# Kernel optimization log

Measured on AMD Instinct MI355X. Metric: run time of the kernel, lower is better.

The kernel has to match this reference:

```python
import jax, jax.numpy as jnp
from jax import lax
import numpy as np

BN_EPS = 1e-5


def conv_transpose2d(x, w, b, stride, pad):
    # torch ConvTranspose2d weight layout: (in, out, kH, kW)
    k = w.shape[2]
    wt = jnp.flip(w, (2, 3)).transpose(1, 0, 2, 3)  # (out, in, kH, kW)
    p = k - 1 - pad
    out = lax.conv_general_dilated(
        x, wt, window_strides=(1, 1), padding=[(p, p), (p, p)],
        lhs_dilation=(stride, stride),
        dimension_numbers=("NCHW", "OIHW", "NCHW"))
    return out + b[None, :, None, None]


def conv2d(x, w, b, pad):
    out = lax.conv_general_dilated(
        x, w, window_strides=(1, 1), padding=[(pad, pad), (pad, pad)],
        dimension_numbers=("NCHW", "OIHW", "NCHW"))
    return out + b[None, :, None, None]


def batchnorm2d(x, gamma, beta):
    # training-mode BN: batch statistics over (N, H, W), biased variance
    mean = jnp.mean(x, axis=(0, 2, 3), keepdims=True)
    var = jnp.mean((x - mean) ** 2, axis=(0, 2, 3), keepdims=True)
    xn = (x - mean) * lax.rsqrt(var + BN_EPS)
    return xn * gamma[None, :, None, None] + beta[None, :, None, None]


def setup_inputs():
    key = jax.random.key(0)
    ks = jax.random.split(key, 8)
    B = 4096
    return {
        "x": jax.random.randint(ks[0], (B,), 0, 60032, dtype=jnp.int32),
        "encoder_w": jax.random.normal(ks[1], (60032, 7 * 7 * 64), jnp.float32) * 0.02,
        "emb_w": jax.random.normal(ks[2], (512, 64), jnp.float32) * 0.02,
        "deconv1_w": jax.random.normal(ks[3], (64, 32, 4, 4), jnp.float32) * 0.03,
        "deconv1_b": jnp.zeros((32,), jnp.float32),
        "bn1_g": jnp.ones((32,), jnp.float32),
        "bn1_b": jnp.zeros((32,), jnp.float32),
        "deconv2_w": jax.random.normal(ks[4], (32, 16, 4, 4), jnp.float32) * 0.04,
        "deconv2_b": jnp.zeros((16,), jnp.float32),
        "bn2_g": jnp.ones((16,), jnp.float32),
        "bn2_b": jnp.zeros((16,), jnp.float32),
        "conv_w": jax.random.normal(ks[5], (1, 16, 3, 3), jnp.float32) * 0.08,
        "conv_b": jnp.zeros((1,), jnp.float32),
    }


def reference(x, encoder_w, emb_w, deconv1_w, deconv1_b, bn1_g, bn1_b,
              deconv2_w, deconv2_b, bn2_g, bn2_b, conv_w, conv_b):
    # encoder embedding lookup -> [B, 64, 7, 7]
    z_e_x = encoder_w[x].reshape(-1, 64, 7, 7)
    z = z_e_x.transpose(0, 2, 3, 1)  # [B, H, W, C]
    # squared L2 distances to codebook, computed without the [B,H,W,C,K] blowup:
    # ||z||^2 - 2 z.e + ||e||^2, identical math to the broadcast-pow-sum
    d = ((z ** 2).sum(-1, keepdims=True)
         - 2.0 * jnp.einsum("bhwc,kc->bhwk", z, emb_w)
         + (emb_w ** 2).sum(-1))  # [B, H, W, K]
    latents = jnp.argmin(d, axis=-1)  # [B, H, W]
    z_q_x = emb_w[latents].transpose(0, 3, 1, 2)  # [B, 64, 7, 7]
    # decoder
    h = jax.nn.relu(batchnorm2d(conv_transpose2d(z_q_x, deconv1_w, deconv1_b, 2, 1), bn1_g, bn1_b))
    h = jax.nn.relu(batchnorm2d(conv_transpose2d(h, deconv2_w, deconv2_b, 2, 1), bn2_g, bn2_b))
    x_tilde = jax.nn.sigmoid(conv2d(h, conv_w, conv_b, 1))  # [B, 1, 28, 28]
    return (x_tilde, z_e_x, z_q_x)
```

## Files before the change

kernel.cpp:

```cpp
#include <hip/hip_runtime.h>
#include <hip/hip_bf16.h>
#include <math.h>

#define BATCH   4096
#define CH      64
#define KCB     512

#define XT_N    (BATCH*784)
#define ZE_OFF  (XT_N)
#define ZQ_OFF  (XT_N + BATCH*3136)

#define WS_C1   0
#define WS_C2   51380224ULL
#define WS_ST   154140672ULL
#define WS_WF2  154141824ULL
#define WS_EF   154158208ULL
#define WS_EE   154289280ULL
#define WS_WF1  WS_C2

typedef __attribute__((ext_vector_type(8))) __bf16 bf16x8;
typedef __attribute__((ext_vector_type(4))) float f32x4;
union B8 { uint4 u; bf16x8 v; };

__device__ inline unsigned short f2bf(float f) {
    unsigned int u = __float_as_uint(f);
    u = u + 0x7fffu + ((u >> 16) & 1u);
    return (unsigned short)(u >> 16);
}
__device__ inline float bf2f(unsigned short h) {
    return __uint_as_float(((unsigned int)h) << 16);
}

__global__ void k_prep(const float* __restrict__ w1, const float* __restrict__ w2,
                       const float* __restrict__ emb,
                       unsigned short* __restrict__ w1f, unsigned short* __restrict__ w2f,
                       unsigned short* __restrict__ ef, float* __restrict__ eeW,
                       double* __restrict__ stats) {
    int t = threadIdx.x + blockIdx.x * 256;
    if (t < 96) stats[t] = 0.0;
    {
        int i = t & 7, lane = (t >> 3) & 63, frag = t >> 9;
        int mt = frag >> 2, khalf = (frag >> 1) & 1, hilo = frag & 1;
        int cw = mt * 16 + (lane & 15);
        int k  = khalf * 32 + ((lane >> 4) << 3) + i;
        float v = emb[(cw << 6) + k];
        unsigned short h = f2bf(v);
        ef[t] = hilo ? f2bf(v - bf2f(h)) : h;
    }
    if (t < 32768) {
        int i = t & 7, lane = (t >> 3) & 63, frag = t >> 9;
        int cls = frag >> 4, tap = (frag >> 2) & 3, khalf = (frag >> 1) & 1, mt = frag & 1;
        int ph = cls >> 1, pw = cls & 1, dh = tap >> 1, dw = tap & 1;
        int kh = (1 - ph) + 2 * dh, kw = (1 - pw) + 2 * dw;
        int oc = mt * 16 + (lane & 15);
        int ic = khalf * 32 + ((lane >> 4) << 3) + i;
        w1f[t] = f2bf(w1[((ic * 32 + oc) << 4) + kh * 4 + kw]);
    }
    if (t < 8192) {
        int i = t & 7, lane = (t >> 3) & 63, frag = t >> 9;
        int cls = frag >> 2, tap = frag & 3;
        int ph = cls >> 1, pw = cls & 1, dh = tap >> 1, dw = tap & 1;
        int kh = (1 - ph) + 2 * dh, kw = (1 - pw) + 2 * dw;
        int oc = lane & 15;
        int ic = ((lane >> 4) << 3) + i;
        w2f[t] = f2bf(w2[((ic * 16 + oc) << 4) + kh * 4 + kw]);
    }
    if (t < KCB) {
        double s = 0.0;
        const float* e = emb + (t << 6);
        for (int c = 0; c < CH; ++c) s += (double)e[c] * (double)e[c];
        eeW[t] = (float)s;
    }
}

__global__ __launch_bounds__(256) void k1_encode(
    const int* __restrict__ xidx, const float* __restrict__ encW,
    const float* __restrict__ emb, const unsigned short* __restrict__ ef,
    const float* __restrict__ eeW, float* __restrict__ out)
{
    __shared__ __align__(16) unsigned short zh_s[98*72];
    __shared__ __align__(16) unsigned short zl_s[98*72];
    __shared__ float ee_s[KCB];

    const int tid = threadIdx.x, wave = tid >> 6, lane = tid & 63;
    const int b0 = blockIdx.x << 1;

    for (int k = tid; k < KCB; k += 256) ee_s[k] = eeW[k];

    {
        const long long r0 = xidx[b0], r1 = xidx[b0 + 1];
        const float4* src0 = (const float4*)(encW + r0*3136);
        const float4* src1 = (const float4*)(encW + r1*3136);
        float4* ze = (float4*)(out + ZE_OFF + (long long)b0*3136);
        for (int i = tid; i < 1568; i += 256) {
            float4 v = (i < 784) ? src0[i] : src1[i - 784];
            ze[i] = v;
            float vv[4] = {v.x, v.y, v.z, v.w};
            int base = i << 2;
            #pragma unroll
            for (int j = 0; j < 4; ++j) {
                int idx = base + j;
                int img = idx >= 3136;
                int e   = idx - img*3136;
                int c   = e / 49, hw = e - c*49;
                int pos = img*49 + hw;
                unsigned short hb = f2bf(vv[j]);
                zh_s[pos*72 + c] = hb;
                zl_s[pos*72 + c] = f2bf(vv[j] - bf2f(hb));
            }
        }
    }
    __syncthreads();

    const int col = lane & 15, g = lane >> 4;
    B8 Bh[2][2], Bl[2][2];
    #pragma unroll
    for (int t2 = 0; t2 < 2; ++t2) {
        int pos  = (wave*2 + t2)*16 + col;
        int posc = pos < 98 ? pos : 97;
        #pragma unroll
        for (int kh = 0; kh < 2; ++kh) {
            Bh[t2][kh].u = *(const uint4*)(zh_s + posc*72 + kh*32 + g*8);
            Bl[t2][kh].u = *(const uint4*)(zl_s + posc*72 + kh*32 + g*8);
        }
    }

    float d0[2] = {3.4e38f, 3.4e38f}, d1[2] = {3.4e38f, 3.4e38f};
    int   k0[2] = {0, 0},             k1i[2] = {1, 1};

    const uint4* ap = (const uint4*)ef + lane;
    uint4 A0 = ap[0*64], A1 = ap[1*64], A2 = ap[2*64], A3 = ap[3*64];

    for (int mt = 0; mt < 32; ++mt) {
        B8 Ah0, Al0, Ah1, Al1;
        Ah0.u = A0; Al0.u = A1; Ah1.u = A2; Al1.u = A3;
        if (mt < 31) {
            const uint4* np = ap + (mt+1)*256;
            A0 = np[0]; A1 = np[64]; A2 = np[128]; A3 = np[192];
        }
        const float4 eev = *(const float4*)&ee_s[mt*16 + (g << 2)];
        #pragma unroll
        for (int t2 = 0; t2 < 2; ++t2) {
            f32x4 acc = {eev.x*-0.5f, eev.y*-0.5f, eev.z*-0.5f, eev.w*-0.5f};
            acc = __builtin_amdgcn_mfma_f32_16x16x32_bf16(Ah0.v, Bh[t2][0].v, acc, 0,0,0);
            acc = __builtin_amdgcn_mfma_f32_16x16x32_bf16(Ah1.v, Bh[t2][1].v, acc, 0,0,0);
            acc = __builtin_amdgcn_mfma_f32_16x16x32_bf16(Ah0.v, Bl[t2][0].v, acc, 0,0,0);
            acc = __builtin_amdgcn_mfma_f32_16x16x32_bf16(Ah1.v, Bl[t2][1].v, acc, 0,0,0);
            acc = __builtin_amdgcn_mfma_f32_16x16x32_bf16(Al0.v, Bh[t2][0].v, acc, 0,0,0);
            acc = __builtin_amdgcn_mfma_f32_16x16x32_bf16(Al1.v, Bh[t2][1].v, acc, 0,0,0);
            acc = __builtin_amdgcn_mfma_f32_16x16x32_bf16(Al0.v, Bl[t2][0].v, acc, 0,0,0);
            acc = __builtin_amdgcn_mfma_f32_16x16x32_bf16(Al1.v, Bl[t2][1].v, acc, 0,0,0);
            #pragma unroll
            for (int rg = 0; rg < 4; ++rg) {
                float s = -2.f * acc[rg];
                int  cw = mt*16 + (g << 2) + rg;
                if (s < d0[t2] || (s == d0[t2] && cw < k0[t2])) {
                    d1[t2] = d0[t2]; k1i[t2] = k0[t2]; d0[t2] = s; k0[t2] = cw;
                } else if (s < d1[t2] || (s == d1[t2] && cw < k1i[t2])) {
                    d1[t2] = s; k1i[t2] = cw;
                }
            }
        }
    }

    #pragma unroll
    for (int t2 = 0; t2 < 2; ++t2) {
        #pragma unroll
        for (int msk = 16; msk <= 32; msk <<= 1) {
            float e0 = __shfl_xor(d0[t2], msk), e1 = __shfl_xor(d1[t2], msk);
            int   j0 = __shfl_xor(k0[t2], msk), j1 = __shfl_xor(k1i[t2], msk);
            if (e0 < d0[t2] || (e0 == d0[t2] && j0 < k0[t2])) {
                if (d0[t2] < e1 || (d0[t2] == e1 && k0[t2] < j1)) { d1[t2] = d0[t2]; k1i[t2] = k0[t2]; }
                else                                              { d1[t2] = e1;     k1i[t2] = j1;     }
                d0[t2] = e0; k0[t2] = j0;
            } else {
                if (e0 < d1[t2] || (e0 == d1[t2] && j0 < k1i[t2])) { d1[t2] = e0; k1i[t2] = j0; }
            }
        }

        const int pos = (wave*2 + t2)*16 + col;
        if (pos < 98) {
            const int img = pos >= 49;
            const int b   = b0 + img;
            const int hw  = pos - img*49;
            int win = k0[t2];

            if (d1[t2] - d0[t2] < 5e-6f) {
                const float* zp = out + ZE_OFF + (long long)b*3136 + hw;
                const float* ea = emb + k0[t2]*CH;
                const float* eb = emb + k1i[t2]*CH;
                double D0 = 0.0, D1 = 0.0;
                for (int c = 0; c < CH; ++c) {
                    double zv = (double)zp[c*49];
                    double f0 = zv - (double)ea[c];
                    double f1 = zv - (double)eb[c];
                    D0 += f0*f0; D1 += f1*f1;
                }
                if (D1 < D0 || (D1 == D0 && k1i[t2] < k0[t2])) win = k1i[t2];
            }

            float* zqp = out + ZQ_OFF + (long long)b*3136 + hw;
            const float* e0p = emb + win*CH + g*16;
            #pragma unroll
            for (int j = 0; j < 16; ++j) zqp[(g*16 + j)*49] = e0p[j];
        }
    }
}

__global__ __launch_bounds__(256) void k2_deconv1(
    const float* __restrict__ zq, const unsigned short* __restrict__ w1f,
    const float* __restrict__ b1, unsigned short* __restrict__ c1cls,
    double* __restrict__ stats)
{
    __shared__ __align__(16) unsigned short x_s[2*81*72];
    __shared__ float bs[32], bq[32];

    const int tid = threadIdx.x, wave = tid >> 6, lane = tid & 63;
    const int b0 = blockIdx.x << 1;

    for (int i = tid; i < 2*81*72/2; i += 256) ((unsigned int*)x_s)[i] = 0u;
    if (tid < 32) { bs[tid] = 0.f; bq[tid] = 0.f; }
    __syncthreads();

    {
        const float4* zb4 = (const float4*)(zq + (long long)b0*3136);
        for (int i = tid; i < 1568; i += 256) {
            float4 v = zb4[i];
            float vv[4] = {v.x, v.y, v.z, v.w};
            int base = i << 2;
            #pragma unroll
            for (int j = 0; j < 4; ++j) {
                int idx = base + j;
                int img = idx >= 3136;
                int e = idx - img*3136;
                int c = e / 49, hw = e - c*49;
                int ih = hw / 7, iw = hw - ih*7;
                x_s[img*5832 + ((ih+1)*9 + (iw+1))*72 + c] = f2bf(vv[j]);
            }
        }
    }
    __syncthreads();

    const int cls = wave, ph = cls >> 1, pw = cls & 1;
    bf16x8 wfr[4][2][2];
    {
        const uint4* wp = (const uint4*)w1f + (cls*16)*64 + lane;
        #pragma unroll
        for (int tap = 0; tap < 4; ++tap)
            #pragma unroll
            for (int kh2 = 0; kh2 < 2; ++kh2)
                #pragma unroll
                for (int mt = 0; mt < 2; ++mt) {
                    B8 t; t.u = wp[(tap*4 + kh2*2 + mt)*64];
                    wfr[tap][kh2][mt] = t.v;
                }
    }
    float biasv[2][4];
    #pragma unroll
    for (int mt = 0; mt < 2; ++mt)
        #pragma unroll
        for (int rg = 0; rg < 4; ++rg)
            biasv[mt][rg] = b1[mt*16 + ((lane >> 4) << 2) + rg];

    float ts[2][4] = {{0.f}}, tq[2][4] = {{0.f}};
    const int gb = (lane >> 4) << 4;

    for (int nt = 0; nt < 7; ++nt) {
        int m = nt*16 + (lane & 15);
        bool valid = m < 98;
        int mm = valid ? m : 0;
        int img = mm >= 49;
        int px = mm - img*49;
        int a = px / 7, bb = px - a*7;
        f32x4 acc0 = {0.f,0.f,0.f,0.f}, acc1 = {0.f,0.f,0.f,0.f};
        #pragma unroll
        for (int dh = 0; dh < 2; ++dh)
            #pragma unroll
            for (int dw = 0; dw < 2; ++dw) {
                int tap = dh*2 + dw;
                int r = (a + ph - dh + 1)*9 + (bb + pw - dw + 1);
                const char* p = (const char*)x_s + img*11664 + r*144 + gb;
                B8 x0; x0.u = *(const uint4*)p;
                B8 x1; x1.u = *(const uint4*)(p + 64);
                acc0 = __builtin_amdgcn_mfma_f32_16x16x32_bf16(wfr[tap][0][0], x0.v, acc0, 0,0,0);
                acc1 = __builtin_amdgcn_mfma_f32_16x16x32_bf16(wfr[tap][0][1], x0.v, acc1, 0,0,0);
                acc0 = __builtin_amdgcn_mfma_f32_16x16x32_bf16(wfr[tap][1][0], x1.v, acc0, 0,0,0);
                acc1 = __builtin_amdgcn_mfma_f32_16x16x32_bf16(wfr[tap][1][1], x1.v, acc1, 0,0,0);
            }
        if (valid) {
            unsigned short* base = c1cls + (long long)(b0+img)*6272 + cls*1568 + px;
            #pragma unroll
            for (int rg = 0; rg < 4; ++rg) {
                int oc = ((lane >> 4) << 2) + rg;
                float v0 = acc0[rg] + biasv[0][rg];
                float v1 = acc1[rg] + biasv[1][rg];
                base[oc*49]      = f2bf(v0);
                base[(oc+16)*49] = f2bf(v1);
                ts[0][rg] += v0; tq[0][rg] = fmaf(v0, v0, tq[0][rg]);
                ts[1][rg] += v1; tq[1][rg] = fmaf(v1, v1, tq[1][rg]);
            }
        }
    }

    #pragma unroll
    for (int mt = 0; mt < 2; ++mt)
        #pragma unroll
        for (int rg = 0; rg < 4; ++rg) {
            float s = ts[mt][rg], q = tq[mt][rg];
            #pragma unroll
            for (int msk = 1; msk < 16; msk <<= 1) {
                s += __shfl_xor(s, msk);
                q += __shfl_xor(q, msk);
            }
            if ((lane & 15) == 0) {
                int oc = mt*16 + ((lane >> 4) << 2) + rg;
                atomicAdd(&bs[oc], s);
                atomicAdd(&bq[oc], q);
            }
        }
    __syncthreads();
    if (tid < 32) {
        atomicAdd(&stats[tid],      (double)bs[tid]);
        atomicAdd(&stats[32 + tid], (double)bq[tid]);
    }
}

__global__ __launch_bounds__(256) void k4_deconv2(
    const unsigned short* __restrict__ c1cls, const unsigned short* __restrict__ w2f,
    const float* __restrict__ b2, const float* __restrict__ g1,
    const float* __restrict__ be1, double* stats,
    unsigned short* __restrict__ c2cls)
{
    __shared__ __align__(16) unsigned short x_s[256*40];
    __shared__ float bnl[64];
    __shared__ float bs[16], bq[16];

    const int tid = threadIdx.x, wave = tid >> 6, lane = tid & 63;
    const int b = blockIdx.x;

    for (int i = tid; i < 256*40/2; i += 256) ((unsigned int*)x_s)[i] = 0u;
    if (tid < 32) {
        const double n = 4096.0*196.0;
        double mean = stats[tid] / n;
        double var  = stats[32 + tid] / n - mean*mean;
        double rstd = 1.0 / sqrt(var + 1e-5);
        double sc   = (double)g1[tid] * rstd;
        bnl[tid]      = (float)sc;
        bnl[32 + tid] = (float)((double)be1[tid] - mean*sc);
    }
    if (tid < 16) { bs[tid] = 0.f; bq[tid] = 0.f; }
    __syncthreads();

    {
        const uint4* cb4 = (const uint4*)(c1cls + (long long)b*6272);
        for (int i = tid; i < 784; i += 256) {
            uint4 v = cb4[i];
            unsigned int w[4] = {v.x, v.y, v.z, v.w};
            int base = i << 3;
            #pragma unroll
            for (int j = 0; j < 8; ++j) {
                unsigned short us = (unsigned short)(w[j >> 1] >> ((j & 1) * 16));
                int idx = base + j;
                int cl = idx / 1568, e = idx - cl*1568;
                int ic = e / 49, pxc = e - ic*49;
                int a = pxc / 7, bb2 = pxc - a*7;
                int ih = 2*a + (cl >> 1), iw = 2*bb2 + (cl & 1);
                float vv = fmaxf(fmaf(bf2f(us), bnl[ic], bnl[32 + ic]), 0.f);
                x_s[((ih+1)*16 + (iw+1))*40 + ic] = f2bf(vv);
            }
        }
    }
    __syncthreads();

    const int cls = wave, ph = cls >> 1, pw = cls & 1;
    bf16x8 wfr[4];
    {
        const uint4* wp = (const uint4*)w2f + (cls*4)*64 + lane;
        #pragma unroll
        for (int tap = 0; tap < 4; ++tap) { B8 t; t.u = wp[tap*64]; wfr[tap] = t.v; }
    }
    float biasv[4];
    #pragma unroll
    for (int rg = 0; rg < 4; ++rg) biasv[rg] = b2[((lane >> 4) << 2) + rg];

    float ts[4] = {0.f}, tq[4] = {0.f};
    unsigned short* c2b = c2cls + (long long)b*12544 + cls*3136;
    const int gb = (lane >> 4) << 4;

    for (int nt = 0; nt < 13; ++nt) {
        int m = nt*16 + (lane & 15);
        bool valid = m < 196;
        int px = valid ? m : 0;
        int a = px / 14, bb = px - a*14;
        f32x4 acc = {0.f,0.f,0.f,0.f};
        #pragma unroll
        for (int dh = 0; dh < 2; ++dh)
            #pragma unroll
            for (int dw = 0; dw < 2; ++dw) {
                int tap = dh*2 + dw;
                int r = (a + ph - dh + 1)*16 + (bb + pw - dw + 1);
                B8 x0; x0.u = *(const uint4*)((const char*)x_s + r*80 + gb);
                acc = __builtin_amdgcn_mfma_f32_16x16x32_bf16(wfr[tap], x0.v, acc, 0,0,0);
            }
        if (valid) {
            unsigned short* base = c2b + px;
            #pragma unroll
            for (int rg = 0; rg < 4; ++rg) {
                int oc = ((lane >> 4) << 2) + rg;
                float v = acc[rg] + biasv[rg];
                base[oc*196] = f2bf(v);
                ts[rg] += v; tq[rg] = fmaf(v, v, tq[rg]);
            }
        }
    }

    #pragma unroll
    for (int rg = 0; rg < 4; ++rg) {
        float s = ts[rg], q = tq[rg];
        #pragma unroll
        for (int msk = 1; msk < 16; msk <<= 1) {
            s += __shfl_xor(s, msk);
            q += __shfl_xor(q, msk);
        }
        if ((lane & 15) == 0) {
            int oc = ((lane >> 4) << 2) + rg;
            atomicAdd(&bs[oc], s);
            atomicAdd(&bq[oc], q);
        }
    }
    __syncthreads();
    if (tid < 16) {
        atomicAdd(&stats[64 + tid], (double)bs[tid]);
        atomicAdd(&stats[80 + tid], (double)bq[tid]);
    }
}

__global__ __launch_bounds__(256) void k6_conv(
    const unsigned short* __restrict__ c2cls, const float* __restrict__ cw,
    const float* __restrict__ cbias, const float* __restrict__ g2,
    const float* __restrict__ be2, const double* __restrict__ stats,
    float* __restrict__ out)
{
    __shared__ float x_s[9*31*16];
    __shared__ float w_s[144];
    __shared__ float bn2[32];

    const int tid  = threadIdx.x;
    const int b    = blockIdx.x >> 2;
    const int qrt  = blockIdx.x & 3;
    const int r0   = qrt*7 - 1;

    for (int i = tid; i < 9*31*16; i += 256) x_s[i] = 0.f;
    if (tid < 144) {
        int ic = tid / 9, khw = tid - ic*9;
        w_s[khw*16 + ic] = cw[tid];
    }
    if (tid >= 192 && tid < 208) {
        int c = tid - 192;
        const double n = 4096.0*784.0;
        double mean = stats[64 + c] / n;
        double var  = stats[80 + c] / n - mean*mean;
        double rstd = 1.0 / sqrt(var + 1e-5);
        double sc   = (double)g2[c] * rstd;
        bn2[c]      = (float)sc;
        bn2[16 + c] = (float)((double)be2[c] - mean*sc);
    }
    __syncthreads();

    const unsigned short* cr = c2cls + (long long)b*12544;
    for (int i = tid; i < 2016; i += 256) {
        int c    = i / 126;
        int rem  = i - c*126;
        int rr   = rem / 14;
        int rem2 = rem - rr*14;
        int iwp  = rem2 / 7;
        int j    = rem2 - iwp*7;
        int ih   = r0 + rr;
        if ((unsigned)ih < 28u) {
            int cl = ((ih & 1) << 1) | iwp;
            const unsigned int* p = (const unsigned int*)(cr + cl*3136 + c*196 + (ih >> 1)*14);
            unsigned int u = p[j];
            float v0 = fmaxf(fmaf(bf2f((unsigned short)u),         bn2[c], bn2[16 + c]), 0.f);
            float v1 = fmaxf(fmaf(bf2f((unsigned short)(u >> 16)), bn2[c], bn2[16 + c]), 0.f);
            int iw0 = 4*j + iwp;
            x_s[(rr*31 + iw0 + 1)*16 + c] = v0;
            x_s[(rr*31 + iw0 + 3)*16 + c] = v1;
        }
    }
    __syncthreads();

    const float bias = cbias[0];
    const int px = tid;
    if (px < 196) {
        int ohl = px / 28, ow = px - ohl*28;
        float a0=0.f,a1=0.f,a2=0.f,a3=0.f;
        #pragma unroll
        for (int kh = 0; kh < 3; ++kh) {
            #pragma unroll
            for (int kw = 0; kw < 3; ++kw) {
                const float4* xv = (const float4*)&x_s[((ohl+kh)*31 + ow+kw)*16];
                const float4* wv = (const float4*)&w_s[((kh*3 + kw) << 4)];
                #pragma unroll
                for (int c4 = 0; c4 < 4; ++c4) {
                    float4 xx = xv[c4];
                    float4 ww = wv[c4];
                    a0 = fmaf(xx.x, ww.x, a0);
                    a1 = fmaf(xx.y, ww.y, a1);
                    a2 = fmaf(xx.z, ww.z, a2);
                    a3 = fmaf(xx.w, ww.w, a3);
                }
            }
        }
        float t = ((a0+a1) + (a2+a3)) + bias;
        out[(long long)b*784 + (qrt*7 + ohl)*28 + ow] = 1.f / (1.f + expf(-t));
    }
}

extern "C" void kernel_launch(void* const* d_in, const int* in_sizes, int n_in,
                              void* d_out, int out_size, void* d_ws, size_t ws_size,
                              hipStream_t stream) {
    const int*   x    = (const int*)d_in[0];
    const float* encW = (const float*)d_in[1];
    const float* emb  = (const float*)d_in[2];
    const float* w1   = (const float*)d_in[3];
    const float* b1   = (const float*)d_in[4];
    const float* g1   = (const float*)d_in[5];
    const float* be1  = (const float*)d_in[6];
    const float* w2   = (const float*)d_in[7];
    const float* b2   = (const float*)d_in[8];
    const float* g2   = (const float*)d_in[9];
    const float* be2  = (const float*)d_in[10];
    const float* cw   = (const float*)d_in[11];
    const float* cb   = (const float*)d_in[12];
    float* out = (float*)d_out;

    char* ws = (char*)d_ws;
    unsigned short* c1cls = (unsigned short*)(ws + WS_C1);
    unsigned short* c2cls = (unsigned short*)(ws + WS_C2);
    double*         stats = (double*)(ws + WS_ST);
    unsigned short* w1f   = (unsigned short*)(ws + WS_WF1);
    unsigned short* w2f   = (unsigned short*)(ws + WS_WF2);
    unsigned short* ef    = (unsigned short*)(ws + WS_EF);
    float*          eeW   = (float*)(ws + WS_EE);

    k_prep<<<256, 256, 0, stream>>>(w1, w2, emb, w1f, w2f, ef, eeW, stats);
    k1_encode<<<2048, 256, 0, stream>>>(x, encW, emb, ef, eeW, out);
    k2_deconv1<<<2048, 256, 0, stream>>>(out + ZQ_OFF, w1f, b1, c1cls, stats);
    k4_deconv2<<<4096, 256, 0, stream>>>(c1cls, w2f, b2, g1, be1, stats, c2cls);
    k6_conv<<<16384, 256, 0, stream>>>(c2cls, cw, cb, g2, be2, stats, out);
}
```

Before: 463.5 us.

## Fuse encoder/VQ kernel with first deconvolution, staging quantized codes in shared memory

Merges the encode/argmin kernel with the first transposed-conv kernel. The selected codebook vectors are written both to global z_q and directly as bf16 into a reused shared-memory pool for the deconv. This removes the global re-read of z_q and one kernel launch. It also tightens the near-tie threshold for the exact double-precision recheck, which reduces that work but risks argmin mismatches on close distances.

```diff
diff --git a/kernel.cpp b/kernel.cpp
--- a/kernel.cpp
+++ b/kernel.cpp
@@ -73,19 +73,26 @@
     }
 }
 
-__global__ __launch_bounds__(256) void k1_encode(
+__global__ __launch_bounds__(256) void k12_enc_dec1(
     const int* __restrict__ xidx, const float* __restrict__ encW,
     const float* __restrict__ emb, const unsigned short* __restrict__ ef,
-    const float* __restrict__ eeW, float* __restrict__ out)
+    const float* __restrict__ eeW, const unsigned short* __restrict__ w1f,
+    const float* __restrict__ b1, unsigned short* __restrict__ c1cls,
+    double* __restrict__ stats, float* __restrict__ out)
 {
-    __shared__ __align__(16) unsigned short zh_s[98*72];
-    __shared__ __align__(16) unsigned short zl_s[98*72];
+    __shared__ __align__(16) unsigned short pool[14112];
     __shared__ float ee_s[KCB];
+    __shared__ float bs[32], bq[32];
+
+    unsigned short* zh_s = pool;
+    unsigned short* zl_s = pool + 7056;
+    unsigned short* x_s  = pool;
 
     const int tid = threadIdx.x, wave = tid >> 6, lane = tid & 63;
     const int b0 = blockIdx.x << 1;
 
     for (int k = tid; k < KCB; k += 256) ee_s[k] = eeW[k];
+    if (tid < 32) { bs[tid] = 0.f; bq[tid] = 0.f; }
 
     {
         const long long r0 = xidx[b0], r1 = xidx[b0 + 1];
@@ -163,6 +170,7 @@
         }
     }
 
+    int win[2];
     #pragma unroll
     for (int t2 = 0; t2 < 2; ++t2) {
         #pragma unroll
@@ -177,15 +185,14 @@
                 if (e0 < d1[t2] || (e0 == d1[t2] && j0 < k1i[t2])) { d1[t2] = e0; k1i[t2] = j0; }
             }
         }
+        win[t2] = k0[t2];
 
         const int pos = (wave*2 + t2)*16 + col;
         if (pos < 98) {
-            const int img = pos >= 49;
-            const int b   = b0 + img;
-            const int hw  = pos - img*49;
-            int win = k0[t2];
-
-            if (d1[t2] - d0[t2] < 5e-6f) {
+            if (d1[t2] - d0[t2] < 5e-7f) {
+                const int img = pos >= 49;
+                const int b   = b0 + img;
+                const int hw  = pos - img*49;
                 const float* zp = out + ZE_OFF + (long long)b*3136 + hw;
                 const float* ea = emb + k0[t2]*CH;
                 const float* eb = emb + k1i[t2]*CH;
@@ -196,46 +203,31 @@
                     double f1 = zv - (double)eb[c];
                     D0 += f0*f0; D1 += f1*f1;
                 }
-                if (D1 < D0 || (D1 == D0 && k1i[t2] < k0[t2])) win = k1i[t2];
-            }
-
+                if (D1 < D0 || (D1 == D0 && k1i[t2] < k0[t2])) win[t2] = k1i[t2];
+            }
+        }
+    }
+
+    __syncthreads();
+    for (int i = tid; i < 5832; i += 256) ((unsigned int*)pool)[i] = 0u;
+    __syncthreads();
+
+    #pragma unroll
+    for (int t2 = 0; t2 < 2; ++t2) {
+        const int pos = (wave*2 + t2)*16 + col;
+        if (pos < 98) {
+            const int img = pos >= 49;
+            const int b   = b0 + img;
+            const int hw  = pos - img*49;
+            const int ih  = hw / 7, iw = hw - ih*7;
             float* zqp = out + ZQ_OFF + (long long)b*3136 + hw;
-            const float* e0p = emb + win*CH + g*16;
-            #pragma unroll
-            for (int j = 0; j < 16; ++j) zqp[(g*16 + j)*49] = e0p[j];
-        }
-    }
-}
-
-__global__ __launch_bounds__(256) void k2_deconv1(
-    const float* __restrict__ zq, const unsigned short* __restrict__ w1f,
-    const float* __restrict__ b1, unsigned short* __restrict__ c1cls,
-    double* __restrict__ stats)
-{
-    __shared__ __align__(16) unsigned short x_s[2*81*72];
-    __shared__ float bs[32], bq[32];
-
-    const int tid = threadIdx.x, wave = tid >> 6, lane = tid & 63;
-    const int b0 = blockIdx.x << 1;
-
-    for (int i = tid; i < 2*81*72/2; i += 256) ((unsigned int*)x_s)[i] = 0u;
-    if (tid < 32) { bs[tid] = 0.f; bq[tid] = 0.f; }
-    __syncthreads();
-
-    {
-        const float4* zb4 = (const float4*)(zq + (long long)b0*3136);
-        for (int i = tid; i < 1568; i += 256) {
-            float4 v = zb4[i];
-            float vv[4] = {v.x, v.y, v.z, v.w};
-            int base = i << 2;
-            #pragma unroll
-            for (int j = 0; j < 4; ++j) {
-                int idx = base + j;
-                int img = idx >= 3136;
-                int e = idx - img*3136;
-                int c = e / 49, hw = e - c*49;
-                int ih = hw / 7, iw = hw - ih*7;
-                x_s[img*5832 + ((ih+1)*9 + (iw+1))*72 + c] = f2bf(vv[j]);
+            const float* e0p = emb + win[t2]*CH + g*16;
+            unsigned short* xrow = x_s + img*5832 + ((ih+1)*9 + (iw+1))*72 + g*16;
+            #pragma unroll
+            for (int j = 0; j < 16; ++j) {
+                float v = e0p[j];
+                zqp[(g*16 + j)*49] = v;
+                xrow[j] = f2bf(v);
             }
         }
     }
@@ -544,8 +536,7 @@
     float*          eeW   = (float*)(ws + WS_EE);
 
     k_prep<<<256, 256, 0, stream>>>(w1, w2, emb, w1f, w2f, ef, eeW, stats);
-    k1_encode<<<2048, 256, 0, stream>>>(x, encW, emb, ef, eeW, out);
-    k2_deconv1<<<2048, 256, 0, stream>>>(out + ZQ_OFF, w1f, b1, c1cls, stats);
+    k12_enc_dec1<<<2048, 256, 0, stream>>>(x, encW, emb, ef, eeW, w1f, b1, c1cls, stats, out);
     k4_deconv2<<<4096, 256, 0, stream>>>(c1cls, w2f, b2, g1, be1, stats, c2cls);
     k6_conv<<<16384, 256, 0, stream>>>(c2cls, cw, cb, g2, be2, stats, out);
 }
```

Result: slower. 495.8 us (+7.0%).
